# Performance work log

Hardware: AMD Instinct MI355X
Metric: run time of the kernel (lower is better)

## Reference

```python
import jax, jax.numpy as jnp
import numpy as np

B, L, G, F = 64, 2048, 512, 3072
N = L + G + F            # nodes per graph
NT = B * N               # total flattened nodes
EG = 16384               # edges per graph (shared topology)
E = B * EG
H, D_IN, NUM_LAYERS = 64, 7, 4
EPS = 1e-5


def setup_inputs() -> dict:
    key = jax.random.key(0)
    ks = jax.random.split(key, 8)
    rng = np.random.default_rng(0)
    x = jax.random.normal(ks[0], (NT, D_IN), jnp.float32)
    # shared topology, replicated per graph with node offsets (PyG batched graph)
    eg = rng.integers(0, N, size=(2, EG))
    offs = (np.arange(B) * N)[None, :, None]
    edge_index = jnp.asarray((eg[:, None, :] + offs).reshape(2, E), dtype=jnp.int32)
    base = np.arange(B)[:, None] * N  # per-graph layout: [loc | gen | line]
    loc_idx = jnp.asarray((base + np.arange(0, L)[None, :]).reshape(-1), jnp.int32)
    prod_idx = jnp.asarray((base + np.arange(L, L + G)[None, :]).reshape(-1), jnp.int32)
    line_idx = jnp.asarray((base + np.arange(L + G, N)[None, :]).reshape(-1), jnp.int32)
    # gen->loc incidence [L, G]: each generator sits at one location
    gm = np.zeros((L, G), np.float32)
    gm[rng.integers(0, L, G), np.arange(G)] = 1.0
    # line->loc signed incidence [L, F]: +1 at from-bus, -1 at to-bus
    lm = np.zeros((L, F), np.float32)
    lm[rng.integers(0, L, F), np.arange(F)] += 1.0
    lm[rng.integers(0, L, F), np.arange(F)] -= 1.0
    s = 1.0 / np.sqrt(H)
    se = 1.0 / np.sqrt(D_IN)
    enc_w = jax.random.uniform(ks[1], (H, D_IN), jnp.float32, -se, se)
    enc_b = jnp.zeros((H,), jnp.float32)
    w_rel = jax.random.uniform(ks[2], (NUM_LAYERS, H, H), jnp.float32, -s, s)
    b_rel = jnp.zeros((NUM_LAYERS, H), jnp.float32)
    w_root = jax.random.uniform(ks[3], (NUM_LAYERS, H, H), jnp.float32, -s, s)
    ln_g = jnp.ones((H,), jnp.float32)
    ln_b = jnp.zeros((H,), jnp.float32)
    prod_w = jax.random.uniform(ks[4], (1, H), jnp.float32, -s, s)
    prod_b = jnp.zeros((1,), jnp.float32)
    flow_w = jax.random.uniform(ks[5], (1, H), jnp.float32, -s, s)
    flow_b = jnp.zeros((1,), jnp.float32)
    return {"x": x, "edge_index": edge_index, "prod_idx": prod_idx,
            "line_idx": line_idx, "loc_idx": loc_idx, "enc_w": enc_w, "enc_b": enc_b,
            "ln_g": ln_g, "ln_b": ln_b, "w_rel": w_rel, "b_rel": b_rel, "w_root": w_root,
            "prod_w": prod_w, "prod_b": prod_b, "flow_w": flow_w, "flow_b": flow_b,
            "gen_mask": jnp.asarray(gm), "line_mask": jnp.asarray(lm)}


def reference(x, edge_index, prod_idx, line_idx, loc_idx, enc_w, enc_b, ln_g, ln_b,
              w_rel, b_rel, w_root, prod_w, prod_b, flow_w, flow_b, gen_mask, line_mask):
    h = jax.nn.relu(x @ enc_w.T + enc_b)                       # [NT, H]
    src, dst = edge_index[0], edge_index[1]
    for i in range(NUM_LAYERS):
        # LayerNorm (shared across layers, as in the torch module)
        mu = jnp.mean(h, axis=-1, keepdims=True)
        var = jnp.mean((h - mu) ** 2, axis=-1, keepdims=True)
        hn = (h - mu) * jax.lax.rsqrt(var + EPS) * ln_g + ln_b
        # GraphConv: W_rel * sum_{j in N(i)} h_j + b_rel + W_root * h_i
        agg = jax.ops.segment_sum(hn[src], dst, num_segments=NT)  # gather + scatter-add
        h = jax.nn.relu(agg @ w_rel[i].T + b_rel[i] + hn @ w_root[i].T)
    p = (h[prod_idx] @ prod_w.T + prod_b).reshape(B, G)
    f = (h[line_idx] @ flow_w.T + flow_b).reshape(B, F)
    demand = x[loc_idx, 0].reshape(B, L)
    md = demand - (p @ gen_mask.T + f @ line_mask.T)           # unmet demand [B, L]
    return (p, f, md)
```

## Files before the change

kernel.cpp:

```cpp
#include <hip/hip_runtime.h>

#define B_ 64
#define L_ 2048
#define G_ 512
#define F_ 3072
#define N_ 5632
#define NT_ 360448
#define EG_ 16384
#define E_ 1048576
#define EPS_ 1e-5f
#define KTOT_ 3584
#define KCH_ 448
#define TCAP_ 384
#define HROW_ 5633

typedef __attribute__((ext_vector_type(8))) short bf8v;
typedef __attribute__((ext_vector_type(4))) float f4v;

__device__ __forceinline__ unsigned short f2bf(float f){
  unsigned int u=__float_as_uint(f);
  unsigned int r=(u + 0x7fffu + ((u>>16)&1u))>>16;
  return (unsigned short)r;
}
__device__ __forceinline__ float bf2f(unsigned short h){
  return __uint_as_float(((unsigned int)h)<<16);
}

__global__ __launch_bounds__(256) void k_prep(const int* __restrict__ ei,
    unsigned short* __restrict__ wcat,
    const float* __restrict__ wrel, const float* __restrict__ wroot,
    int* __restrict__ offT, int* __restrict__ srcs2,
    const float* __restrict__ x, const int* __restrict__ loci, float* __restrict__ outmd,
    unsigned short* __restrict__ hn, unsigned short* __restrict__ hnb,
    const float* __restrict__ ew, const float* __restrict__ eb,
    const float* __restrict__ lng, const float* __restrict__ lnb){
  int bid=blockIdx.x, tid=threadIdx.x;
  if(bid>=600){
    int lane=tid&63, wid=tid>>6;
    int idx=bid-600;
    int gid=idx/88;
    int nb0=(idx%88)*64 + wid*16;
    int ng=lane>>4;
    int lig=lane&15;
    float w[4][7], bias[4], gam[4], bet[4];
    #pragma unroll
    for(int j=0;j<4;j++){
      int c=lig*4+j;
      #pragma unroll
      for(int k=0;k<7;k++) w[j][k]=ew[c*7+k];
      bias[j]=eb[c]; gam[j]=lng[c]; bet[j]=lnb[c];
    }
    #pragma unroll
    for(int t=0;t<4;t++){
      int n=nb0 + t*4 + ng;
      long xrow=((long)gid*N_+n)*7;
      float xv[7];
      #pragma unroll
      for(int k=0;k<7;k++) xv[k]=x[xrow+k];
      float h[4]; float s1=0.f, s2=0.f;
      #pragma unroll
      for(int j=0;j<4;j++){
        float a=bias[j];
        #pragma unroll
        for(int k=0;k<7;k++) a+=xv[k]*w[j][k];
        a=fmaxf(a,0.f);
        h[j]=a; s1+=a; s2+=a*a;
      }
      #pragma unroll
      for(int o=1;o<16;o<<=1){ s1+=__shfl_xor(s1,o,64); s2+=__shfl_xor(s2,o,64); }
      float mu=s1*(1.f/64.f);
      float var=s2*(1.f/64.f)-mu*mu;
      float inv=rsqrtf(var+EPS_);
      unsigned int p0=(unsigned int)f2bf((h[0]-mu)*inv*gam[0]+bet[0])
                    | ((unsigned int)f2bf((h[1]-mu)*inv*gam[1]+bet[1])<<16);
      unsigned int p1=(unsigned int)f2bf((h[2]-mu)*inv*gam[2]+bet[2])
                    | ((unsigned int)f2bf((h[3]-mu)*inv*gam[3]+bet[3])<<16);
      *(uint2*)(hn + (size_t)n*4096 + gid*64 + lig*4) = (uint2){p0,p1};
    }
    return;
  }
  if(bid>=88){
    int i=(bid-88)*256+tid;
    if(i<B_*L_) outmd[i]=x[(long)loci[i]*7];
    if(i<32768){
      int l=i>>13; int rest=i&8191; int n=rest>>7; int k=rest&127;
      float v=(k<64)? wrel[((long)l*64+n)*64+k] : wroot[((long)l*64+n)*64+(k-64)];
      wcat[i]=f2bf(v);
    }
    if(i<4096){
      hn [(size_t)N_*4096+i]=0;
      hnb[(size_t)N_*4096+i]=0;
    }
    return;
  }
  __shared__ int cnt64[64], cur64[64];
  int nb=bid*64;
  if(tid<64) cnt64[tid]=0;
  __syncthreads();
  for(int e=tid;e<EG_;e+=1024){
    int d0=ei[E_+e], d1=ei[E_+e+256], d2=ei[E_+e+512], d3=ei[E_+e+768];
    unsigned t0=(unsigned)(d0-nb), t1=(unsigned)(d1-nb);
    unsigned t2=(unsigned)(d2-nb), t3=(unsigned)(d3-nb);
    if(t0<64u) atomicAdd(&cnt64[t0],1);
    if(t1<64u) atomicAdd(&cnt64[t1],1);
    if(t2<64u) atomicAdd(&cnt64[t2],1);
    if(t3<64u) atomicAdd(&cnt64[t3],1);
  }
  __syncthreads();
  if(tid<64){
    int v=cnt64[tid];
    int vo=__shfl_xor(v,1,64);
    int c0=(tid&1)? vo : v;
    int psum=v+vo;
    int ppad=(psum+3)&~3;
    int wv=(tid&1)? 0 : ppad;
    int s=wv;
    #pragma unroll
    for(int o=1;o<64;o<<=1){ int u=__shfl_up(s,o,64); if(tid>=o) s+=u; }
    int pairstart=s-ppad;
    int nst=pairstart + ((tid&1)? c0 : 0);
    offT[bid*65+tid]=nst;
    cur64[tid]=nst;
    if(tid==63) offT[bid*65+64]=s;
    if(!(tid&1)){
      int dw=N_ | ((nb+tid)<<16);
      for(int q=psum;q<ppad;q++){
        int p=pairstart+q;
        if(p<TCAP_) srcs2[bid*TCAP_+p]=dw;
      }
    }
  }
  __syncthreads();
  for(int e=tid;e<EG_;e+=1024){
    int s0=ei[e],    s1=ei[e+256],    s2=ei[e+512],    s3=ei[e+768];
    int d0=ei[E_+e], d1=ei[E_+e+256], d2=ei[E_+e+512], d3=ei[E_+e+768];
    unsigned t0=(unsigned)(d0-nb), t1=(unsigned)(d1-nb);
    unsigned t2=(unsigned)(d2-nb), t3=(unsigned)(d3-nb);
    if(t0<64u){ int p=atomicAdd(&cur64[t0],1); if(p<TCAP_) srcs2[bid*TCAP_+p]=s0|(d0<<16); }
    if(t1<64u){ int p=atomicAdd(&cur64[t1],1); if(p<TCAP_) srcs2[bid*TCAP_+p]=s1|(d1<<16); }
    if(t2<64u){ int p=atomicAdd(&cur64[t2],1); if(p<TCAP_) srcs2[bid*TCAP_+p]=s2|(d2<<16); }
    if(t3<64u){ int p=atomicAdd(&cur64[t3],1); if(p<TCAP_) srcs2[bid*TCAP_+p]=s3|(d3<<16); }
  }
}

__device__ __forceinline__ void upadd(float* a, uint4 qa, uint4 qb){
  unsigned int t[8]={qa.x,qa.y,qa.z,qa.w,qb.x,qb.y,qb.z,qb.w};
  #pragma unroll
  for(int j=0;j<8;j++){
    a[2*j]   += __uint_as_float(t[j]<<16);
    a[2*j+1] += __uint_as_float(t[j]&0xffff0000u);
  }
}

__device__ __forceinline__ void stw16(char* base, int r, int chunk, unsigned int p0,
                                      unsigned int p1, unsigned int p2, unsigned int p3){
  int byte = r*128 + chunk*16;
  byte ^= (r&7)<<4;
  *(uint4*)(base + byte) = (uint4){p0,p1,p2,p3};
}
__device__ __forceinline__ bf8v ld16(const char* base, int r, int chunk){
  int byte = r*128 + chunk*16;
  byte ^= (r&7)<<4;
  return *(const bf8v*)(base + byte);
}

__global__ __launch_bounds__(256,6) void k_layer(const unsigned short* __restrict__ hs,
    unsigned short* __restrict__ hd, const int* __restrict__ offT, const int* __restrict__ srcs2,
    const unsigned short* __restrict__ wcat, const float* __restrict__ brel,
    const float* __restrict__ lng, const float* __restrict__ lnb, int do_ln){
  __shared__ uint4 aggl4[1024];
  char* agglc=(char*)aggl4;
  int tid=threadIdx.x;
  int w=tid>>6, lane=tid&63;
  int dst0=blockIdx.x*2;

  {
    int jj=dst0>>6, loc=dst0&63;
    int kb=offT[jj*65+loc];
    int ke=offT[jj*65+loc+2];
    const int* esp=srcs2 + jj*TCAP_;
    int co=tid*16;
    float aA[16], aB[16];
    #pragma unroll
    for(int c=0;c<16;c++){ aA[c]=0.f; aB[c]=0.f; }
    for(int k=kb;k<ke;k+=4){
      int u0=esp[k], u1=esp[k+1], u2=esp[k+2], u3=esp[k+3];
      const unsigned short* r0=hs+(size_t)(u0&0xffff)*4096+co;
      const unsigned short* r1=hs+(size_t)(u1&0xffff)*4096+co;
      const unsigned short* r2=hs+(size_t)(u2&0xffff)*4096+co;
      const unsigned short* r3=hs+(size_t)(u3&0xffff)*4096+co;
      uint4 qa0=*(const uint4*)r0, qb0=*(const uint4*)(r0+8);
      uint4 qa1=*(const uint4*)r1, qb1=*(const uint4*)(r1+8);
      uint4 qa2=*(const uint4*)r2, qb2=*(const uint4*)(r2+8);
      uint4 qa3=*(const uint4*)r3, qb3=*(const uint4*)(r3+8);
      if((u0>>16)==dst0) upadd(aA,qa0,qb0); else upadd(aB,qa0,qb0);
      if((u1>>16)==dst0) upadd(aA,qa1,qb1); else upadd(aB,qa1,qb1);
      if((u2>>16)==dst0) upadd(aA,qa2,qb2); else upadd(aB,qa2,qb2);
      if((u3>>16)==dst0) upadd(aA,qa3,qb3); else upadd(aB,qa3,qb3);
    }
    unsigned int pA[8], pB[8];
    #pragma unroll
    for(int j=0;j<8;j++){
      pA[j]=(unsigned int)f2bf(aA[2*j]) | ((unsigned int)f2bf(aA[2*j+1])<<16);
      pB[j]=(unsigned int)f2bf(aB[2*j]) | ((unsigned int)f2bf(aB[2*j+1])<<16);
    }
    int rl=tid>>2, c2=(tid&3)*2;
    stw16(agglc, rl,    c2,   pA[0],pA[1],pA[2],pA[3]);
    stw16(agglc, rl,    c2+1, pA[4],pA[5],pA[6],pA[7]);
    stw16(agglc, 64+rl, c2,   pB[0],pB[1],pB[2],pB[3]);
    stw16(agglc, 64+rl, c2+1, pB[4],pB[5],pB[6],pB[7]);
  }
  __syncthreads();

  int m=lane&15, quad=lane>>4;
  f4v acc[2][4];
  float bias_nt[4], g_nt[4], b_nt[4];
  #pragma unroll
  for(int nt=0;nt<4;nt++){
    int c=nt*16+m;
    bias_nt[nt]=brel[c];
    g_nt[nt]=lng[c]; b_nt[nt]=lnb[c];
    acc[0][nt]=(f4v){0.f,0.f,0.f,0.f};
    acc[1][nt]=(f4v){0.f,0.f,0.f,0.f};
  }
  #pragma unroll
  for(int mt=0;mt<2;mt++){
    int R=w*32+mt*16+m;
    bf8v af0=ld16(agglc,R,quad);
    bf8v af1=ld16(agglc,R,4+quad);
    int dn=dst0+(R>>6), gg=R&63;
    const unsigned short* hrow=hs+(size_t)dn*4096+gg*64;
    bf8v af2=*(const bf8v*)(hrow+quad*8);
    bf8v af3=*(const bf8v*)(hrow+32+quad*8);
    #pragma unroll
    for(int nt=0;nt<4;nt++){
      const unsigned short* wrow=wcat + (long)(nt*16+m)*128 + quad*8;
      bf8v b0=*(const bf8v*)(wrow);
      bf8v b1=*(const bf8v*)(wrow+32);
      bf8v b2=*(const bf8v*)(wrow+64);
      bf8v b3=*(const bf8v*)(wrow+96);
      acc[mt][nt]=__builtin_amdgcn_mfma_f32_16x16x32_bf16(af0,b0,acc[mt][nt],0,0,0);
      acc[mt][nt]=__builtin_amdgcn_mfma_f32_16x16x32_bf16(af1,b1,acc[mt][nt],0,0,0);
      acc[mt][nt]=__builtin_amdgcn_mfma_f32_16x16x32_bf16(af2,b2,acc[mt][nt],0,0,0);
      acc[mt][nt]=__builtin_amdgcn_mfma_f32_16x16x32_bf16(af3,b3,acc[mt][nt],0,0,0);
    }
  }
  #pragma unroll
  for(int mt=0;mt<2;mt++){
    float v[4][4];
    #pragma unroll
    for(int nt=0;nt<4;nt++)
      #pragma unroll
      for(int r=0;r<4;r++)
        v[nt][r]=fmaxf(acc[mt][nt][r]+bias_nt[nt],0.f);
    if(do_ln){
      #pragma unroll
      for(int r=0;r<4;r++){
        float rs=v[0][r]+v[1][r]+v[2][r]+v[3][r];
        float rss=v[0][r]*v[0][r]+v[1][r]*v[1][r]+v[2][r]*v[2][r]+v[3][r]*v[3][r];
        #pragma unroll
        for(int o=1;o<16;o<<=1){ rs+=__shfl_xor(rs,o,64); rss+=__shfl_xor(rss,o,64); }
        float mu=rs*(1.f/64.f);
        float var=rss*(1.f/64.f)-mu*mu;
        float inv=rsqrtf(var+EPS_);
        #pragma unroll
        for(int nt=0;nt<4;nt++) v[nt][r]=(v[nt][r]-mu)*inv*g_nt[nt]+b_nt[nt];
      }
    }
    #pragma unroll
    for(int r=0;r<4;r++){
      int R=w*32+mt*16+quad*4+r;
      int dn=dst0+(R>>6), gg=R&63;
      unsigned short* out=hd + (size_t)dn*4096 + gg*64;
      #pragma unroll
      for(int nt=0;nt<4;nt++) out[nt*16+m]=f2bf(v[nt][r]);
    }
  }
}

__global__ __launch_bounds__(256) void k_readout2(const unsigned short* __restrict__ h,
    const int* __restrict__ prodi, const int* __restrict__ linei,
    const float* __restrict__ pw, const float* __restrict__ pb,
    const float* __restrict__ fw, const float* __restrict__ fb,
    float* __restrict__ outp, float* __restrict__ outf,
    unsigned short* __restrict__ pfhi, unsigned short* __restrict__ pflo){
  int i=blockIdx.x*256+threadIdx.x;
  const int MP=B_*G_;
  const int MT=MP+B_*F_;
  if(i>=MT) return;
  bool isp=i<MP;
  int j=isp? i : i-MP;
  unsigned nf=(unsigned)(isp? prodi[j] : linei[j]);
  unsigned gg=nf/(unsigned)N_;
  unsigned node=nf-gg*(unsigned)N_;
  const float* wv=isp? pw:fw;
  float acc=isp? pb[0]:fb[0];
  const uint4* hp=(const uint4*)(h + (size_t)node*4096 + gg*64);
  #pragma unroll
  for(int c=0;c<8;c++){
    uint4 u=hp[c];
    unsigned int uu[4]={u.x,u.y,u.z,u.w};
    #pragma unroll
    for(int q=0;q<4;q++){
      float lo=__uint_as_float(uu[q]<<16);
      float hi=__uint_as_float(uu[q]&0xffff0000u);
      acc += lo*wv[c*8+2*q] + hi*wv[c*8+2*q+1];
    }
  }
  int b,kcol;
  if(isp){ outp[j]=acc; b=j/G_; kcol=j%G_; }
  else   { outf[j]=acc; b=j/F_; kcol=G_+j%F_; }
  unsigned short hi=f2bf(acc);
  pfhi[(long)b*KTOT_+kcol]=hi;
  pflo[(long)b*KTOT_+kcol]=f2bf(acc-bf2f(hi));
}

__global__ __launch_bounds__(256) void k_md_gemm(const float* __restrict__ gm, const float* __restrict__ lm,
    const unsigned short* __restrict__ pfhi, const unsigned short* __restrict__ pflo,
    float* __restrict__ outmd){
  int tid=threadIdx.x;
  int w=tid>>6, lane=tid&63;
  int m=lane&15, quad=lane>>4;
  int lb=blockIdx.x>>3, kc=blockIdx.x&7;
  int l=lb*64 + w*16 + m;
  f4v acc[4];
  #pragma unroll
  for(int nt=0;nt<4;nt++) acc[nt]=(f4v){0.f,0.f,0.f,0.f};
  int kk0=kc*KCH_;
  for(int s=0;s<KCH_/32;s++){
    int kk=kk0+s*32;
    const float* ap = (kk<G_)? gm + (long)l*G_ + kk : lm + (long)l*F_ + (kk-G_);
    float4 a0=*(const float4*)(ap+quad*8);
    float4 a1=*(const float4*)(ap+quad*8+4);
    bf8v af;
    af[0]=(short)f2bf(a0.x); af[1]=(short)f2bf(a0.y);
    af[2]=(short)f2bf(a0.z); af[3]=(short)f2bf(a0.w);
    af[4]=(short)f2bf(a1.x); af[5]=(short)f2bf(a1.y);
    af[6]=(short)f2bf(a1.z); af[7]=(short)f2bf(a1.w);
    #pragma unroll
    for(int nt=0;nt<4;nt++){
      int b=nt*16+m;
      const unsigned short* bp=pfhi + (long)b*KTOT_ + kk + quad*8;
      const unsigned short* lp=pflo + (long)b*KTOT_ + kk + quad*8;
      bf8v bh=*(const bf8v*)bp;
      bf8v bl=*(const bf8v*)lp;
      acc[nt]=__builtin_amdgcn_mfma_f32_16x16x32_bf16(af,bh,acc[nt],0,0,0);
      acc[nt]=__builtin_amdgcn_mfma_f32_16x16x32_bf16(af,bl,acc[nt],0,0,0);
    }
  }
  int lrow=lb*64 + w*16 + quad*4;
  #pragma unroll
  for(int r=0;r<4;r++)
    #pragma unroll
    for(int nt=0;nt<4;nt++)
      atomicAdd(&outmd[(long)(nt*16+m)*L_ + lrow+r], -acc[nt][r]);
}

extern "C" void kernel_launch(void* const* d_in, const int* in_sizes, int n_in,
                              void* d_out, int out_size, void* d_ws, size_t ws_size,
                              hipStream_t stream){
  const float* x    =(const float*)d_in[0];
  const int*   ei   =(const int*)d_in[1];
  const int*   prodi=(const int*)d_in[2];
  const int*   linei=(const int*)d_in[3];
  const int*   loci =(const int*)d_in[4];
  const float* ew   =(const float*)d_in[5];
  const float* eb   =(const float*)d_in[6];
  const float* lng  =(const float*)d_in[7];
  const float* lnb  =(const float*)d_in[8];
  const float* wrel =(const float*)d_in[9];
  const float* brel =(const float*)d_in[10];
  const float* wroot=(const float*)d_in[11];
  const float* pw   =(const float*)d_in[12];
  const float* pb   =(const float*)d_in[13];
  const float* fw   =(const float*)d_in[14];
  const float* fb   =(const float*)d_in[15];
  const float* gm   =(const float*)d_in[16];
  const float* lm   =(const float*)d_in[17];

  char* ws=(char*)d_ws;
  unsigned short* hnA =(unsigned short*)ws;
  unsigned short* hnB =hnA + (size_t)HROW_*4096;
  unsigned short* wcat=hnB + (size_t)HROW_*4096;
  unsigned short* pfhi=wcat + 32768;
  unsigned short* pflo=pfhi + (size_t)B_*KTOT_;
  int* offT =(int*)(pflo + (size_t)B_*KTOT_);
  int* srcs2=offT + 88*65;

  float* outp =(float*)d_out;
  float* outf =outp + (size_t)B_*G_;
  float* outmd=outf + (size_t)B_*F_;

  k_prep<<<600+NT_/64,256,0,stream>>>(ei,wcat,wrel,wroot,offT,srcs2,
                                      x,loci,outmd,hnA,hnB,ew,eb,lng,lnb);
  for(int i=0;i<4;i++){
    const unsigned short* hs=(i&1)?hnB:hnA;
    unsigned short* hd=(i&1)?hnA:hnB;
    k_layer<<<N_/2,256,0,stream>>>(hs,hd,offT,srcs2,wcat+(size_t)i*8192,
        brel+(size_t)i*64,lng,lnb,(i<3)?1:0);
  }
  {
    int MT=B_*(G_+F_);
    k_readout2<<<(MT+255)/256,256,0,stream>>>(hnA,prodi,linei,pw,pb,fw,fb,outp,outf,pfhi,pflo);
  }
  k_md_gemm<<<256,256,0,stream>>>(gm,lm,pfhi,pflo,outmd);
}
```

Baseline: 432.9 us.

## Retile GraphConv layer by node tiles and graph-chunks with XCD-aware block mapping

Each block of the layer kernel used to handle 2 destination nodes across all 64 graphs. It now handles 32 destination nodes for a chunk of 4 graphs. Block IDs are mapped so that each XCD owns a fixed set of graph chunks, which is meant to keep source-row gathers within that XCD's L2. Output is staged through shared memory and written with coalesced 16-byte stores instead of scattered 2-byte stores. The cost is narrower 8-byte gathers per lane and an extra synchronisation.

```diff
diff --git a/kernel.cpp b/kernel.cpp
--- a/kernel.cpp
+++ b/kernel.cpp
@@ -143,20 +143,10 @@
   }
 }
 
-__device__ __forceinline__ void upadd(float* a, uint4 qa, uint4 qb){
-  unsigned int t[8]={qa.x,qa.y,qa.z,qa.w,qb.x,qb.y,qb.z,qb.w};
-  #pragma unroll
-  for(int j=0;j<8;j++){
-    a[2*j]   += __uint_as_float(t[j]<<16);
-    a[2*j+1] += __uint_as_float(t[j]&0xffff0000u);
-  }
-}
-
-__device__ __forceinline__ void stw16(char* base, int r, int chunk, unsigned int p0,
-                                      unsigned int p1, unsigned int p2, unsigned int p3){
-  int byte = r*128 + chunk*16;
+__device__ __forceinline__ void stw8(char* base, int r, int c8, unsigned int p0, unsigned int p1){
+  int byte = r*128 + c8*8;
   byte ^= (r&7)<<4;
-  *(uint4*)(base + byte) = (uint4){p0,p1,p2,p3};
+  *(uint2*)(base + byte) = (uint2){p0,p1};
 }
 __device__ __forceinline__ bf8v ld16(const char* base, int r, int chunk){
   int byte = r*128 + chunk*16;
@@ -172,43 +162,74 @@
   char* agglc=(char*)aggl4;
   int tid=threadIdx.x;
   int w=tid>>6, lane=tid&63;
-  int dst0=blockIdx.x*2;
+  int bid=blockIdx.x;
+  int xcd=bid&7, bq=bid>>3;
+  int chunk=xcd + 8*(bq/176);
+  int tile =bq%176;
+  int n0t=tile*32;
+  int cb=chunk*256;
 
   {
-    int jj=dst0>>6, loc=dst0&63;
-    int kb=offT[jj*65+loc];
-    int ke=offT[jj*65+loc+2];
+    int jj=n0t>>6;
+    int loc0=(n0t&63)+w*8;
     const int* esp=srcs2 + jj*TCAP_;
-    int co=tid*16;
-    float aA[16], aB[16];
-    #pragma unroll
-    for(int c=0;c<16;c++){ aA[c]=0.f; aB[c]=0.f; }
-    for(int k=kb;k<ke;k+=4){
-      int u0=esp[k], u1=esp[k+1], u2=esp[k+2], u3=esp[k+3];
-      const unsigned short* r0=hs+(size_t)(u0&0xffff)*4096+co;
-      const unsigned short* r1=hs+(size_t)(u1&0xffff)*4096+co;
-      const unsigned short* r2=hs+(size_t)(u2&0xffff)*4096+co;
-      const unsigned short* r3=hs+(size_t)(u3&0xffff)*4096+co;
-      uint4 qa0=*(const uint4*)r0, qb0=*(const uint4*)(r0+8);
-      uint4 qa1=*(const uint4*)r1, qb1=*(const uint4*)(r1+8);
-      uint4 qa2=*(const uint4*)r2, qb2=*(const uint4*)(r2+8);
-      uint4 qa3=*(const uint4*)r3, qb3=*(const uint4*)(r3+8);
-      if((u0>>16)==dst0) upadd(aA,qa0,qb0); else upadd(aB,qa0,qb0);
-      if((u1>>16)==dst0) upadd(aA,qa1,qb1); else upadd(aB,qa1,qb1);
-      if((u2>>16)==dst0) upadd(aA,qa2,qb2); else upadd(aB,qa2,qb2);
-      if((u3>>16)==dst0) upadd(aA,qa3,qb3); else upadd(aB,qa3,qb3);
-    }
-    unsigned int pA[8], pB[8];
-    #pragma unroll
-    for(int j=0;j<8;j++){
-      pA[j]=(unsigned int)f2bf(aA[2*j]) | ((unsigned int)f2bf(aA[2*j+1])<<16);
-      pB[j]=(unsigned int)f2bf(aB[2*j]) | ((unsigned int)f2bf(aB[2*j+1])<<16);
-    }
-    int rl=tid>>2, c2=(tid&3)*2;
-    stw16(agglc, rl,    c2,   pA[0],pA[1],pA[2],pA[3]);
-    stw16(agglc, rl,    c2+1, pA[4],pA[5],pA[6],pA[7]);
-    stw16(agglc, 64+rl, c2,   pB[0],pB[1],pB[2],pB[3]);
-    stw16(agglc, 64+rl, c2+1, pB[4],pB[5],pB[6],pB[7]);
+    const int* offp=offT + jj*65;
+    int g=lane>>4, c4=lane&15;
+    int cw=cb + g*64 + c4*4;
+    #pragma unroll
+    for(int p=0;p<4;p++){
+      int loc=loc0+p*2;
+      int dstA=jj*64+loc;
+      int kb=offp[loc], ke=offp[loc+2];
+      float aA0=0.f,aA1=0.f,aA2=0.f,aA3=0.f;
+      float aB0=0.f,aB1=0.f,aB2=0.f,aB3=0.f;
+      for(int k=kb;k<ke;k+=4){
+        int u0=esp[k], u1=esp[k+1], u2=esp[k+2], u3=esp[k+3];
+        const unsigned short* r0=hs+(size_t)(u0&0xffff)*4096+cw;
+        const unsigned short* r1=hs+(size_t)(u1&0xffff)*4096+cw;
+        const unsigned short* r2=hs+(size_t)(u2&0xffff)*4096+cw;
+        const unsigned short* r3=hs+(size_t)(u3&0xffff)*4096+cw;
+        uint2 e0=*(const uint2*)r0;
+        uint2 e1=*(const uint2*)r1;
+        uint2 e2=*(const uint2*)r2;
+        uint2 e3=*(const uint2*)r3;
+        if((u0>>16)==dstA){
+          aA0+=__uint_as_float(e0.x<<16); aA1+=__uint_as_float(e0.x&0xffff0000u);
+          aA2+=__uint_as_float(e0.y<<16); aA3+=__uint_as_float(e0.y&0xffff0000u);
+        }else{
+          aB0+=__uint_as_float(e0.x<<16); aB1+=__uint_as_float(e0.x&0xffff0000u);
+          aB2+=__uint_as_float(e0.y<<16); aB3+=__uint_as_float(e0.y&0xffff0000u);
+        }
+        if((u1>>16)==dstA){
+          aA0+=__uint_as_float(e1.x<<16); aA1+=__uint_as_float(e1.x&0xffff0000u);
+          aA2+=__uint_as_float(e1.y<<16); aA3+=__uint_as_float(e1.y&0xffff0000u);
+        }else{
+          aB0+=__uint_as_float(e1.x<<16); aB1+=__uint_as_float(e1.x&0xffff0000u);
+          aB2+=__uint_as_float(e1.y<<16); aB3+=__uint_as_float(e1.y&0xffff0000u);
+        }
+        if((u2>>16)==dstA){
+          aA0+=__uint_as_float(e2.x<<16); aA1+=__uint_as_float(e2.x&0xffff0000u);
+          aA2+=__uint_as_float(e2.y<<16); aA3+=__uint_as_float(e2.y&0xffff0000u);
+        }else{
+          aB0+=__uint_as_float(e2.x<<16); aB1+=__uint_as_float(e2.x&0xffff0000u);
+          aB2+=__uint_as_float(e2.y<<16); aB3+=__uint_as_float(e2.y&0xffff0000u);
+        }
+        if((u3>>16)==dstA){
+          aA0+=__uint_as_float(e3.x<<16); aA1+=__uint_as_float(e3.x&0xffff0000u);
+          aA2+=__uint_as_float(e3.y<<16); aA3+=__uint_as_float(e3.y&0xffff0000u);
+        }else{
+          aB0+=__uint_as_float(e3.x<<16); aB1+=__uint_as_float(e3.x&0xffff0000u);
+          aB2+=__uint_as_float(e3.y<<16); aB3+=__uint_as_float(e3.y&0xffff0000u);
+        }
+      }
+      int ln=w*8+p*2;
+      stw8(agglc, ln*4+g,     c4,
+           (unsigned int)f2bf(aA0) | ((unsigned int)f2bf(aA1)<<16),
+           (unsigned int)f2bf(aA2) | ((unsigned int)f2bf(aA3)<<16));
+      stw8(agglc, (ln+1)*4+g, c4,
+           (unsigned int)f2bf(aB0) | ((unsigned int)f2bf(aB1)<<16),
+           (unsigned int)f2bf(aB2) | ((unsigned int)f2bf(aB3)<<16));
+    }
   }
   __syncthreads();
 
@@ -228,8 +249,8 @@
     int R=w*32+mt*16+m;
     bf8v af0=ld16(agglc,R,quad);
     bf8v af1=ld16(agglc,R,4+quad);
-    int dn=dst0+(R>>6), gg=R&63;
-    const unsigned short* hrow=hs+(size_t)dn*4096+gg*64;
+    int dn=n0t+(R>>2), gg=R&3;
+    const unsigned short* hrow=hs+(size_t)dn*4096+cb+gg*64;
     bf8v af2=*(const bf8v*)(hrow+quad*8);
     bf8v af3=*(const bf8v*)(hrow+32+quad*8);
     #pragma unroll
@@ -245,6 +266,9 @@
       acc[mt][nt]=__builtin_amdgcn_mfma_f32_16x16x32_bf16(af3,b3,acc[mt][nt],0,0,0);
     }
   }
+  __syncthreads();
+  unsigned short* ot=(unsigned short*)agglc;
+
   #pragma unroll
   for(int mt=0;mt<2;mt++){
     float v[4][4];
@@ -270,10 +294,20 @@
     #pragma unroll
     for(int r=0;r<4;r++){
       int R=w*32+mt*16+quad*4+r;
-      int dn=dst0+(R>>6), gg=R&63;
-      unsigned short* out=hd + (size_t)dn*4096 + gg*64;
-      #pragma unroll
-      for(int nt=0;nt<4;nt++) out[nt*16+m]=f2bf(v[nt][r]);
+      #pragma unroll
+      for(int nt=0;nt<4;nt++) ot[R*64 + nt*16+m]=f2bf(v[nt][r]);
+    }
+  }
+  __syncthreads();
+
+  {
+    int segoff=(tid&31)*8;
+    int nd0=tid>>5;
+    #pragma unroll
+    for(int nn=0;nn<4;nn++){
+      int node=nd0+nn*8;
+      uint4 val=*(const uint4*)(ot + node*256 + segoff);
+      *(uint4*)(hd + (size_t)(n0t+node)*4096 + cb + segoff) = val;
     }
   }
 }
@@ -396,7 +430,7 @@
   for(int i=0;i<4;i++){
     const unsigned short* hs=(i&1)?hnB:hnA;
     unsigned short* hd=(i&1)?hnA:hnB;
-    k_layer<<<N_/2,256,0,stream>>>(hs,hd,offT,srcs2,wcat+(size_t)i*8192,
+    k_layer<<<16*176,256,0,stream>>>(hs,hd,offT,srcs2,wcat+(size_t)i*8192,
         brel+(size_t)i*64,lng,lnb,(i<3)?1:0);
   }
   {
```

After: 414.6 us. 1.04x faster.
